# Kernel optimization log

Hardware: AMD Instinct MI355X
Metric: run time of the kernel (lower is better)

## Reference

```python
import jax, jax.numpy as jnp
import numpy as np
import math

N = 8192
D = 512

def setup_inputs() -> dict:
    key = jax.random.key(0)
    k1, k2, k3, k4, k5 = jax.random.split(key, 5)
    x = jax.random.normal(k1, (N, D), dtype=jnp.float32)
    mask = jax.random.randint(k2, (N, N), 0, 2) == 1
    s = 1.0 / math.sqrt(D)
    Wq = jax.random.normal(k3, (D, D), dtype=jnp.float32) * s
    Wk = jax.random.normal(k4, (D, D), dtype=jnp.float32) * s
    Wv = jax.random.normal(k5, (D, D), dtype=jnp.float32) * s
    return {"x": x, "mask": mask, "Wq": Wq, "Wk": Wk, "Wv": Wv}

def reference(x, mask, Wq, Wk, Wv):
    d_model = x.shape[-1]
    # torch nn.Linear: y = x @ W^T
    Q = x @ Wq.T
    K = x @ Wk.T
    V = x @ Wv.T
    scores = (Q @ K.T) / jnp.sqrt(jnp.asarray(d_model, x.dtype))  # [N, N]
    scores = jnp.where(mask, jnp.asarray(-1e9, x.dtype), scores)
    # manual stable softmax, matching the original op sequence
    scores = jnp.exp(scores - jnp.max(scores, axis=1, keepdims=True))
    attn = scores / jnp.sum(scores, axis=-1, keepdims=True)
    cntx = attn @ V
    return (cntx, attn)
```

## Files before the change

### kernel.cpp

```cpp
#include <hip/hip_runtime.h>

#define NTOK 8192
#define DMODEL 512
#define NWORDS 128
#define ESTRIDE (2 * NTOK)

typedef _Float16 f16;
typedef _Float16 f16x4 __attribute__((ext_vector_type(4)));
typedef _Float16 f16x8 __attribute__((ext_vector_type(8)));
typedef float f32x4 __attribute__((ext_vector_type(4)));
typedef unsigned long long u64;

__device__ __forceinline__ void async_ld16(const void* g, void* l) {
  __builtin_amdgcn_global_load_lds((const __attribute__((address_space(1))) void*)g,
                                   (__attribute__((address_space(3))) void*)l, 16, 0, 0);
}

__global__ void pack_f16(const float* __restrict__ s, f16* __restrict__ d, int n) {
  int i = (blockIdx.x * 256 + threadIdx.x) * 4;
  if (i >= n) return;
  float4 v = *(const float4*)(s + i);
  f16x4 h; h.x = (f16)v.x; h.y = (f16)v.y; h.z = (f16)v.z; h.w = (f16)v.w;
  *(f16x4*)(d + i) = h;
}

__global__ __launch_bounds__(256) void pack_mask(const int* __restrict__ mask,
                                                 u64* __restrict__ bits) {
  int wave = (blockIdx.x * 256 + threadIdx.x) >> 6;
  int lane = threadIdx.x & 63;
  size_t W0 = (size_t)wave * 8;
#pragma unroll
  for (int i = 0; i < 8; ++i) {
    int m = __builtin_nontemporal_load(mask + (W0 + i) * 64 + lane);
    u64 b = __ballot(m != 0);
    if (lane == 0) bits[W0 + i] = b;
  }
}

__global__ __launch_bounds__(256) void transpose_f16(const f16* __restrict__ src,
                                                     f16* __restrict__ dst) {
  __shared__ f16 T[64][72];
  int t = threadIdx.x;
  int tok0 = blockIdx.x * 64, d0 = blockIdx.y * 64;
#pragma unroll
  for (int i = 0; i < 2; ++i) {
    int row = (t >> 3) + i * 32;
    int col = (t & 7) * 8;
    f16x8 v = *(const f16x8*)(src + (size_t)(tok0 + row) * DMODEL + d0 + col);
    *(f16x8*)(&T[row][col]) = v;
  }
  __syncthreads();
#pragma unroll
  for (int i = 0; i < 2; ++i) {
    int od = (t >> 3) + i * 32;
    int ot = (t & 7) * 8;
    f16x8 v;
#pragma unroll
    for (int j = 0; j < 8; ++j) v[j] = T[ot + j][od];
    *(f16x8*)(dst + (size_t)(d0 + od) * NTOK + tok0 + ot) = v;
  }
}

__device__ __forceinline__ void stage128x32(const f16* G, int r0, int k0, int rs,
                                            f16* lds, int t) {
  int wv = t >> 6;
  int srcsw = (((t & 3) ^ ((t >> 2) & 3)) * 8);
  const f16* g = G + (size_t)(r0 + (t >> 2)) * rs + k0 + srcsw;
  async_ld16(g, (char*)lds + wv * 1024);
  async_ld16(g + (size_t)64 * rs, (char*)lds + 4096 + wv * 1024);
}

template <int RS>
__device__ __forceinline__ void gemm128(const f16* A, const f16* B, int m0, int n0,
                                        f16* As, f16* Bs, int t, f32x4 (&acc)[4][4]) {
  int lane = t & 63, quad = lane >> 4, l15 = lane & 15, wv = t >> 6;
  int m_off = (wv & 1) * 64, n_off = (wv >> 1) * 64;
  int sl = (quad ^ (l15 & 3)) * 8;
  stage128x32(A, m0, 0, RS, As, t);
  stage128x32(B, n0, 0, RS, Bs, t);
  __syncthreads();
  for (int kt = 0; kt < RS; kt += 32) {
    int cur = (kt >> 5) & 1;
    if (kt + 32 < RS) {
      stage128x32(A, m0, kt + 32, RS, As + (cur ^ 1) * 4096, t);
      stage128x32(B, n0, kt + 32, RS, Bs + (cur ^ 1) * 4096, t);
    }
    const f16* Ac = As + cur * 4096;
    const f16* Bc = Bs + cur * 4096;
    f16x8 af[4], bf[4];
#pragma unroll
    for (int mt = 0; mt < 4; ++mt)
      af[mt] = *(const f16x8*)(Ac + (m_off + mt * 16 + l15) * 32 + sl);
#pragma unroll
    for (int nt = 0; nt < 4; ++nt)
      bf[nt] = *(const f16x8*)(Bc + (n_off + nt * 16 + l15) * 32 + sl);
#pragma unroll
    for (int mt = 0; mt < 4; ++mt)
#pragma unroll
      for (int nt = 0; nt < 4; ++nt)
        acc[mt][nt] = __builtin_amdgcn_mfma_f32_16x16x32_f16(af[mt], bf[nt], acc[mt][nt], 0, 0, 0);
    __syncthreads();
  }
}

__global__ __launch_bounds__(256) void qkv_gemm(const f16* __restrict__ X,
                                                const f16* __restrict__ Wall,
                                                f16* __restrict__ Out) {
  __shared__ f16 As[2 * 128 * 32];
  __shared__ f16 Bs[2 * 128 * 32];
  int t = threadIdx.x;
  int z = blockIdx.z;
  const f16* B = Wall + (size_t)z * DMODEL * DMODEL;
  f16* C = Out + (size_t)z * NTOK * DMODEL;
  int m0 = blockIdx.y * 128, n0 = blockIdx.x * 128;
  int lane = t & 63, wv = t >> 6, quad = lane >> 4, l15 = lane & 15;
  int m_off = (wv & 1) * 64, n_off = (wv >> 1) * 64;
  f32x4 acc[4][4] = {};
  gemm128<DMODEL>(X, B, m0, n0, As, Bs, t, acc);
#pragma unroll
  for (int mt = 0; mt < 4; ++mt)
#pragma unroll
    for (int nt = 0; nt < 4; ++nt)
#pragma unroll
      for (int r = 0; r < 4; ++r) {
        int row = m0 + m_off + mt * 16 + quad * 4 + r;
        int col = n0 + n_off + nt * 16 + l15;
        C[(size_t)row * DMODEL + col] = (f16)acc[mt][nt][r];
      }
}

__global__ __launch_bounds__(256) void scores2(const f16* __restrict__ Q,
                                               const f16* __restrict__ Kh,
                                               const u64* __restrict__ bits,
                                               f16* __restrict__ Eh,
                                               float* __restrict__ rowsum) {
  __shared__ f16 SM[128 * 128];
  f16* As = SM;
  f16* Bs = SM + 8192;
  int t = threadIdx.x;
  int orig = blockIdx.x + (blockIdx.y << 6);
  int wg = (orig & 7) * 512 + (orig >> 3);
  int m0 = (((wg >> 9) * 8 + (wg & 7))) * 128;
  int n0 = ((wg >> 3) & 63) * 128;
  int lane = t & 63, wv = t >> 6, quad = lane >> 4, l15 = lane & 15;
  int m_off = (wv & 1) * 64, n_off = (wv >> 1) * 64;
  f32x4 acc[4][4] = {};
  gemm128<DMODEL>(Q, Kh, m0, n0, As, Bs, t, acc);
  const float scale = 0.044194173824159216f;
#pragma unroll
  for (int mt = 0; mt < 4; ++mt)
#pragma unroll
    for (int r = 0; r < 4; ++r) {
      int lrow = m_off + mt * 16 + quad * 4 + r;
      int row = m0 + lrow;
      u64 w = bits[(size_t)row * NWORDS + ((n0 + n_off) >> 6)];
      float rs = 0.f;
#pragma unroll
      for (int nt = 0; nt < 4; ++nt) {
        float s = acc[mt][nt][r] * scale;
        float e = ((w >> (nt * 16 + l15)) & 1) ? 0.f : __expf(s);
        rs += e;
        int col = n_off + nt * 16 + l15;
        int phys = (((col >> 3) ^ (lrow & 15)) << 3) | (col & 7);
        SM[lrow * 128 + phys] = (f16)e;
      }
      rs += __shfl_xor(rs, 1);
      rs += __shfl_xor(rs, 2);
      rs += __shfl_xor(rs, 4);
      rs += __shfl_xor(rs, 8);
      if (l15 == 0) atomicAdd(&rowsum[row], rs);
    }
  __syncthreads();
#pragma unroll
  for (int p = 0; p < 8; ++p) {
    int lrow = p * 16 + (t >> 4);
    int cb = t & 15;
    f16x8 v = *(const f16x8*)(SM + lrow * 128 + ((cb ^ (lrow & 15)) << 3));
    *(f16x8*)(Eh + (size_t)(m0 + lrow) * ESTRIDE + n0 + cb * 8) = v;
  }
}

__device__ __forceinline__ void stage_pv(const f16* __restrict__ Eh,
                                         const f16* __restrict__ Vt, int r0, int kt,
                                         f16* Es, f16* Vs, int t) {
  int wv = t >> 6;
  int srcsw = (((t & 3) ^ ((t >> 2) & 3)) * 8);
  async_ld16(Eh + (size_t)(r0 + (t >> 2)) * ESTRIDE + kt + srcsw, (char*)Es + wv * 1024);
#pragma unroll
  for (int i = 0; i < 4; ++i)
    async_ld16(Vt + (size_t)(i * 128 + (t >> 2)) * NTOK + kt + srcsw,
               (char*)Vs + i * 8192 + wv * 1024);
}

__global__ __launch_bounds__(512, 2) void pv_kernel(const f16* __restrict__ Eh,
                                                    const float* __restrict__ rowsum,
                                                    const f16* __restrict__ Vt,
                                                    float* __restrict__ cntx) {
  __shared__ f16 Es[2][128 * 32];
  __shared__ f16 Vs[2][512 * 32];
  int t = threadIdx.x;
  int orig = blockIdx.x + (blockIdx.y << 6);
  int wg = (orig & 7) * 32 + (orig >> 3);
  int r0 = (wg & 63) * 128;
  int k0 = (wg >> 6) * 2048;
  int lane = t & 63, wv = t >> 6, quad = lane >> 4, l15 = lane & 15;
  int m_off = (wv & 1) * 64, n_off = (wv >> 1) * 128;
  int sl2 = (quad ^ (l15 & 3)) * 8;
  f32x4 acc[4][8] = {};
  stage_pv(Eh, Vt, r0, k0, Es[0], Vs[0], t);
  __syncthreads();
  for (int i = 0; i < 64; ++i) {
    int cur = i & 1;
    if (i < 63) stage_pv(Eh, Vt, r0, k0 + (i + 1) * 32, Es[cur ^ 1], Vs[cur ^ 1], t);
    const f16* Ec = Es[cur];
    const f16* Vc = Vs[cur];
    f16x8 af[4], bf[8];
#pragma unroll
    for (int mt = 0; mt < 4; ++mt)
      af[mt] = *(const f16x8*)(Ec + (m_off + mt * 16 + l15) * 32 + sl2);
#pragma unroll
    for (int nt = 0; nt < 8; ++nt)
      bf[nt] = *(const f16x8*)(Vc + (n_off + nt * 16 + l15) * 32 + sl2);
#pragma unroll
    for (int mt = 0; mt < 4; ++mt)
#pragma unroll
      for (int nt = 0; nt < 8; ++nt)
        acc[mt][nt] = __builtin_amdgcn_mfma_f32_16x16x32_f16(af[mt], bf[nt], acc[mt][nt], 0, 0, 0);
    __syncthreads();
  }
#pragma unroll
  for (int mt = 0; mt < 4; ++mt)
#pragma unroll
    for (int r = 0; r < 4; ++r) {
      int row = r0 + m_off + mt * 16 + quad * 4 + r;
      float ri = 1.0f / rowsum[row];
#pragma unroll
      for (int nt = 0; nt < 8; ++nt) {
        int col = n_off + nt * 16 + l15;
        atomicAdd(&cntx[(size_t)row * DMODEL + col], acc[mt][nt][r] * ri);
      }
    }
}

__global__ __launch_bounds__(256) void expand_attn(float* __restrict__ attn,
                                                   const float* __restrict__ rowsum) {
  int t = threadIdx.x;
  int wv = t >> 6, lane = t & 63;
  int row = blockIdx.x * 4 + wv;
  float ri = 1.0f / rowsum[row];
  const f16* src = (const f16*)(attn + (size_t)row * NTOK);
  float* dst = attn + (size_t)row * NTOK;
  f16x8 v0, v1, v2, v3, v4, v5, v6, v7, v8, v9, va, vb, vc, vd, ve, vf;
#define LD(i, reg) reg = __builtin_nontemporal_load((const f16x8*)(src + (i) * 512 + lane * 8))
  LD(0, v0); LD(1, v1); LD(2, v2); LD(3, v3); LD(4, v4); LD(5, v5); LD(6, v6); LD(7, v7);
  LD(8, v8); LD(9, v9); LD(10, va); LD(11, vb); LD(12, vc); LD(13, vd); LD(14, ve); LD(15, vf);
#undef LD
  asm volatile("" ::: "memory");
#define ST(i, reg)                                                            \
  {                                                                           \
    f32x4 lo, hi;                                                             \
    lo.x = (float)reg[0] * ri; lo.y = (float)reg[1] * ri;                     \
    lo.z = (float)reg[2] * ri; lo.w = (float)reg[3] * ri;                     \
    hi.x = (float)reg[4] * ri; hi.y = (float)reg[5] * ri;                     \
    hi.z = (float)reg[6] * ri; hi.w = (float)reg[7] * ri;                     \
    __builtin_nontemporal_store(lo, (f32x4*)(dst + (i) * 512 + lane * 8));    \
    __builtin_nontemporal_store(hi, (f32x4*)(dst + (i) * 512 + lane * 8 + 4)); \
  }
  ST(0, v0); ST(1, v1); ST(2, v2); ST(3, v3); ST(4, v4); ST(5, v5); ST(6, v6); ST(7, v7);
  ST(8, v8); ST(9, v9); ST(10, va); ST(11, vb); ST(12, vc); ST(13, vd); ST(14, ve); ST(15, vf);
#undef ST
}

extern "C" void kernel_launch(void* const* d_in, const int* in_sizes, int n_in,
                              void* d_out, int out_size, void* d_ws, size_t ws_size,
                              hipStream_t stream) {
  const float* x  = (const float*)d_in[0];
  const int* mask = (const int*)d_in[1];
  const float* Wq = (const float*)d_in[2];
  const float* Wk = (const float*)d_in[3];
  const float* Wv = (const float*)d_in[4];
  float* cntx = (float*)d_out;
  float* attn = (float*)d_out + (size_t)NTOK * DMODEL;

  f16* xh = (f16*)d_ws;
  f16* Wh = xh + (size_t)NTOK * DMODEL;
  f16* QKV = Wh + (size_t)3 * DMODEL * DMODEL;
  f16* Qh = QKV;
  f16* Kh = QKV + (size_t)NTOK * DMODEL;
  f16* Vh = QKV + (size_t)2 * NTOK * DMODEL;
  f16* Vt = QKV + (size_t)3 * NTOK * DMODEL;
  float* rowsum = (float*)(Vt + (size_t)NTOK * DMODEL);

  u64* bits = (u64*)cntx;
  f16* Eh = (f16*)attn;

  hipMemsetAsync(rowsum, 0, NTOK * sizeof(float), stream);

  pack_f16<<<dim3(NTOK * DMODEL / 1024), 256, 0, stream>>>(x, xh, NTOK * DMODEL);
  pack_f16<<<dim3(DMODEL * DMODEL / 1024), 256, 0, stream>>>(Wq, Wh, DMODEL * DMODEL);
  pack_f16<<<dim3(DMODEL * DMODEL / 1024), 256, 0, stream>>>(Wk, Wh + DMODEL * DMODEL, DMODEL * DMODEL);
  pack_f16<<<dim3(DMODEL * DMODEL / 1024), 256, 0, stream>>>(Wv, Wh + 2 * DMODEL * DMODEL, DMODEL * DMODEL);
  pack_mask<<<dim3(NTOK * NWORDS / 8 / 4), 256, 0, stream>>>(mask, bits);

  qkv_gemm<<<dim3(DMODEL / 128, NTOK / 128, 3), 256, 0, stream>>>(xh, Wh, QKV);
  transpose_f16<<<dim3(NTOK / 64, DMODEL / 64), 256, 0, stream>>>(Vh, Vt);
  scores2<<<dim3(NTOK / 128, NTOK / 128), 256, 0, stream>>>(Qh, Kh, bits, Eh, rowsum);

  hipMemsetAsync(cntx, 0, (size_t)NTOK * DMODEL * sizeof(float), stream);
  pv_kernel<<<dim3(NTOK / 128, 4), 512, 0, stream>>>(Eh, rowsum, Vt, cntx);
  expand_attn<<<dim3(NTOK / 4), 256, 0, stream>>>(attn, rowsum);
}
```

Before: 871.3 us.

## Fuse attention normalization into PV kernel, move unnormalized scores to workspace

Unnormalized f16 exponentials now go to a compact workspace buffer instead of being staged inside the attn output, and the PV kernel writes the normalized fp32 attn tile from its LDS-staged E chunks while it accumulates P·V. This removes the separate expand_attn pass, which re-read the f16 data and rewrote the fp32 matrix. The block-to-tile mapping changes to a one-dimensional grid that spreads the four K chunks across row tiles. The mask bits move to the workspace, so the cntx memset can happen up front. In exchange the PV kernel's inner loop carries extra LDS reads and large global stores that may compete with the MFMA work, and the workspace must be large enough for the N×N f16 buffer.

```diff
diff --git a/kernel.cpp b/kernel.cpp
--- a/kernel.cpp
+++ b/kernel.cpp
@@ -3,7 +3,6 @@
 #define NTOK 8192
 #define DMODEL 512
 #define NWORDS 128
-#define ESTRIDE (2 * NTOK)
 
 typedef _Float16 f16;
 typedef _Float16 f16x4 __attribute__((ext_vector_type(4)));
@@ -176,7 +175,7 @@
     int lrow = p * 16 + (t >> 4);
     int cb = t & 15;
     f16x8 v = *(const f16x8*)(SM + lrow * 128 + ((cb ^ (lrow & 15)) << 3));
-    *(f16x8*)(Eh + (size_t)(m0 + lrow) * ESTRIDE + n0 + cb * 8) = v;
+    *(f16x8*)(Eh + (size_t)(m0 + lrow) * NTOK + n0 + cb * 8) = v;
   }
 }
 
@@ -185,27 +184,31 @@
                                          f16* Es, f16* Vs, int t) {
   int wv = t >> 6;
   int srcsw = (((t & 3) ^ ((t >> 2) & 3)) * 8);
-  async_ld16(Eh + (size_t)(r0 + (t >> 2)) * ESTRIDE + kt + srcsw, (char*)Es + wv * 1024);
+  async_ld16(Eh + (size_t)(r0 + (t >> 2)) * NTOK + kt + srcsw, (char*)Es + wv * 1024);
 #pragma unroll
   for (int i = 0; i < 4; ++i)
     async_ld16(Vt + (size_t)(i * 128 + (t >> 2)) * NTOK + kt + srcsw,
                (char*)Vs + i * 8192 + wv * 1024);
 }
 
-__global__ __launch_bounds__(512, 2) void pv_kernel(const f16* __restrict__ Eh,
-                                                    const float* __restrict__ rowsum,
-                                                    const f16* __restrict__ Vt,
-                                                    float* __restrict__ cntx) {
+__global__ __launch_bounds__(512, 2) void pv_fused(const f16* __restrict__ Eh,
+                                                   const float* __restrict__ rowsum,
+                                                   const f16* __restrict__ Vt,
+                                                   float* __restrict__ cntx,
+                                                   float* __restrict__ attn) {
   __shared__ f16 Es[2][128 * 32];
   __shared__ f16 Vs[2][512 * 32];
   int t = threadIdx.x;
-  int orig = blockIdx.x + (blockIdx.y << 6);
-  int wg = (orig & 7) * 32 + (orig >> 3);
-  int r0 = (wg & 63) * 128;
-  int k0 = (wg >> 6) * 2048;
+  int orig = blockIdx.x;
+  int chunk = orig & 3;
+  int r0 = (((orig >> 2) + chunk * 16) & 63) * 128;
+  int k0 = chunk * 2048;
   int lane = t & 63, wv = t >> 6, quad = lane >> 4, l15 = lane & 15;
   int m_off = (wv & 1) * 64, n_off = (wv >> 1) * 128;
   int sl2 = (quad ^ (l15 & 3)) * 8;
+  int arow = t >> 2;
+  int aslot = (t & 3) ^ (arow & 3);
+  float rinv = 1.0f / rowsum[r0 + arow];
   f32x4 acc[4][8] = {};
   stage_pv(Eh, Vt, r0, k0, Es[0], Vs[0], t);
   __syncthreads();
@@ -214,6 +217,17 @@
     if (i < 63) stage_pv(Eh, Vt, r0, k0 + (i + 1) * 32, Es[cur ^ 1], Vs[cur ^ 1], t);
     const f16* Ec = Es[cur];
     const f16* Vc = Vs[cur];
+    {
+      f16x8 ev = *(const f16x8*)(Ec + t * 8);
+      f32x4 lo, hi;
+      lo.x = (float)ev[0] * rinv; lo.y = (float)ev[1] * rinv;
+      lo.z = (float)ev[2] * rinv; lo.w = (float)ev[3] * rinv;
+      hi.x = (float)ev[4] * rinv; hi.y = (float)ev[5] * rinv;
+      hi.z = (float)ev[6] * rinv; hi.w = (float)ev[7] * rinv;
+      float* ap = attn + (size_t)(r0 + arow) * NTOK + k0 + i * 32 + aslot * 8;
+      __builtin_nontemporal_store(lo, (f32x4*)ap);
+      __builtin_nontemporal_store(hi, (f32x4*)(ap + 4));
+    }
     f16x8 af[4], bf[8];
 #pragma unroll
     for (int mt = 0; mt < 4; ++mt)
@@ -240,35 +254,6 @@
         atomicAdd(&cntx[(size_t)row * DMODEL + col], acc[mt][nt][r] * ri);
       }
     }
-}
-
-__global__ __launch_bounds__(256) void expand_attn(float* __restrict__ attn,
-                                                   const float* __restrict__ rowsum) {
-  int t = threadIdx.x;
-  int wv = t >> 6, lane = t & 63;
-  int row = blockIdx.x * 4 + wv;
-  float ri = 1.0f / rowsum[row];
-  const f16* src = (const f16*)(attn + (size_t)row * NTOK);
-  float* dst = attn + (size_t)row * NTOK;
-  f16x8 v0, v1, v2, v3, v4, v5, v6, v7, v8, v9, va, vb, vc, vd, ve, vf;
-#define LD(i, reg) reg = __builtin_nontemporal_load((const f16x8*)(src + (i) * 512 + lane * 8))
-  LD(0, v0); LD(1, v1); LD(2, v2); LD(3, v3); LD(4, v4); LD(5, v5); LD(6, v6); LD(7, v7);
-  LD(8, v8); LD(9, v9); LD(10, va); LD(11, vb); LD(12, vc); LD(13, vd); LD(14, ve); LD(15, vf);
-#undef LD
-  asm volatile("" ::: "memory");
-#define ST(i, reg)                                                            \
-  {                                                                           \
-    f32x4 lo, hi;                                                             \
-    lo.x = (float)reg[0] * ri; lo.y = (float)reg[1] * ri;                     \
-    lo.z = (float)reg[2] * ri; lo.w = (float)reg[3] * ri;                     \
-    hi.x = (float)reg[4] * ri; hi.y = (float)reg[5] * ri;                     \
-    hi.z = (float)reg[6] * ri; hi.w = (float)reg[7] * ri;                     \
-    __builtin_nontemporal_store(lo, (f32x4*)(dst + (i) * 512 + lane * 8));    \
-    __builtin_nontemporal_store(hi, (f32x4*)(dst + (i) * 512 + lane * 8 + 4)); \
-  }
-  ST(0, v0); ST(1, v1); ST(2, v2); ST(3, v3); ST(4, v4); ST(5, v5); ST(6, v6); ST(7, v7);
-  ST(8, v8); ST(9, v9); ST(10, va); ST(11, vb); ST(12, vc); ST(13, vd); ST(14, ve); ST(15, vf);
-#undef ST
 }
 
 extern "C" void kernel_launch(void* const* d_in, const int* in_sizes, int n_in,
@@ -290,11 +275,11 @@
   f16* Vh = QKV + (size_t)2 * NTOK * DMODEL;
   f16* Vt = QKV + (size_t)3 * NTOK * DMODEL;
   float* rowsum = (float*)(Vt + (size_t)NTOK * DMODEL);
-
-  u64* bits = (u64*)cntx;
-  f16* Eh = (f16*)attn;
+  f16* Eh = (f16*)(rowsum + NTOK);
+  u64* bits = (u64*)(Eh + (size_t)NTOK * NTOK);
 
   hipMemsetAsync(rowsum, 0, NTOK * sizeof(float), stream);
+  hipMemsetAsync(cntx, 0, (size_t)NTOK * DMODEL * sizeof(float), stream);
 
   pack_f16<<<dim3(NTOK * DMODEL / 1024), 256, 0, stream>>>(x, xh, NTOK * DMODEL);
   pack_f16<<<dim3(DMODEL * DMODEL / 1024), 256, 0, stream>>>(Wq, Wh, DMODEL * DMODEL);
@@ -305,8 +290,5 @@
   qkv_gemm<<<dim3(DMODEL / 128, NTOK / 128, 3), 256, 0, stream>>>(xh, Wh, QKV);
   transpose_f16<<<dim3(NTOK / 64, DMODEL / 64), 256, 0, stream>>>(Vh, Vt);
   scores2<<<dim3(NTOK / 128, NTOK / 128), 256, 0, stream>>>(Qh, Kh, bits, Eh, rowsum);
-
-  hipMemsetAsync(cntx, 0, (size_t)NTOK * DMODEL * sizeof(float), stream);
-  pv_kernel<<<dim3(NTOK / 128, 4), 512, 0, stream>>>(Eh, rowsum, Vt, cntx);
-  expand_attn<<<dim3(NTOK / 4), 256, 0, stream>>>(attn, rowsum);
-}
+  pv_fused<<<dim3(256), 512, 0, stream>>>(Eh, rowsum, Vt, cntx, attn);
+}
```

Result: faster. 808.4 us (-7.2%).
